# Kernel optimization log

Measured on AMD Instinct MI355X. Metric: run time of the kernel, lower is better.

Reference implementation:

```python
import jax, jax.numpy as jnp
import numpy as np

DIM = 1024
NUM_HEADS = 16
HEAD_DIM = DIM // NUM_HEADS
SCALE = HEAD_DIM ** -0.5


def setup_inputs() -> dict:
    key = jax.random.key(0)
    k1, k2, k3, k4 = jax.random.split(key, 4)
    x = jax.random.normal(k1, (4, 2048, DIM), dtype=jnp.float32)
    # torch nn.Linear(dim, 3*dim, bias=False): weight shape [3*dim, dim]
    w_qkv = jax.random.normal(k2, (3 * DIM, DIM), dtype=jnp.float32) * (DIM ** -0.5)
    # torch nn.Linear(dim, dim): weight [dim, dim], bias [dim]
    w_proj = jax.random.normal(k3, (DIM, DIM), dtype=jnp.float32) * (DIM ** -0.5)
    b_proj = jax.random.normal(k4, (DIM,), dtype=jnp.float32) * 0.01
    return {"x": x, "w_qkv": w_qkv, "w_proj": w_proj, "b_proj": b_proj}


def reference(x, w_qkv, w_proj, b_proj):
    B, N, C = x.shape
    # qkv: [B, N, 3*C] -> [3, B, H, N, Dh]
    qkv = (x @ w_qkv.T).reshape(B, N, 3, NUM_HEADS, HEAD_DIM)
    qkv = jnp.transpose(qkv, (2, 0, 3, 1, 4))
    q, k, v = qkv[0], qkv[1], qkv[2]
    # full score matrix, as in the original module
    attn = jnp.einsum("bhqd,bhkd->bhqk", q, k) * SCALE
    attn = jax.nn.softmax(attn, axis=-1)
    out = jnp.einsum("bhqk,bhkd->bhqd", attn, v)  # [B,H,N,Dh]
    out = jnp.transpose(out, (0, 2, 1, 3)).reshape(B, N, C)
    return out @ w_proj.T + b_proj
```

## Files before the change

### kernel.cpp

```cpp
#include <hip/hip_runtime.h>
#include <stdint.h>

#define DIM 1024
#define SEQ 2048
#define BATCH 4
#define ROWS (BATCH*SEQ)
#define QSCALE 0.1803368801111f

typedef __attribute__((ext_vector_type(8))) short bf16x8;
typedef __attribute__((ext_vector_type(4))) float f32x4;

#if __has_builtin(__builtin_amdgcn_exp2f)
#define EXP2F(x) __builtin_amdgcn_exp2f(x)
#else
#define EXP2F(x) __expf((x) * 0.69314718056f)
#endif

__device__ __forceinline__ unsigned short f2bf(float f) {
  union { float f; unsigned int u; } v; v.f = f;
  unsigned int u = v.u;
  return (unsigned short)((u + 0x7FFFu + ((u >> 16) & 1u)) >> 16);
}

__device__ __forceinline__ unsigned int pack_bf16_trunc(float lo, float hi) {
  union { float f; unsigned int u; } a, b;
  a.f = lo; b.f = hi;
  return __builtin_amdgcn_perm(b.u, a.u, 0x07060302u);
}

__device__ __forceinline__ void gload_lds16(const void* g, void* l) {
  __builtin_amdgcn_global_load_lds(
      (const __attribute__((address_space(1))) unsigned int*)g,
      (__attribute__((address_space(3))) unsigned int*)l,
      16, 0, 0);
}

__global__ void cast_f32_bf16(const float* __restrict__ src,
                              unsigned short* __restrict__ dst, int n) {
  int i = (blockIdx.x * blockDim.x + threadIdx.x) * 4;
  if (i < n) {
    float4 f = *(const float4*)(src + i);
    ushort4 o;
    o.x = f2bf(f.x); o.y = f2bf(f.y); o.z = f2bf(f.z); o.w = f2bf(f.w);
    *(ushort4*)(dst + i) = o;
  }
}

__global__ __launch_bounds__(256) void gemm_qkv(
    const unsigned short* __restrict__ A,
    const unsigned short* __restrict__ W,
    unsigned short* __restrict__ qb,
    unsigned short* __restrict__ kb,
    unsigned short* __restrict__ vtb) {
  const int K = DIM;
  __shared__ unsigned short Al[128 * 32];
  __shared__ unsigned short Wl[128 * 32];
  const int tid  = threadIdx.x;
  const int wave = tid >> 6, lane = tid & 63;
  const int quad = lane >> 4, l16 = lane & 15;
  const int m0 = blockIdx.y * 128, n0 = blockIdx.x * 128;
  const int wr = (wave >> 1) * 64, wc = (wave & 1) * 64;

  f32x4 acc[4][4];
#pragma unroll
  for (int i = 0; i < 4; i++)
#pragma unroll
    for (int j = 0; j < 4; j++) acc[i][j] = (f32x4)0.f;

  const int arow = wave * 16 + (lane >> 2);
  const int acol = (lane & 3) * 8;
  const unsigned short* Ag = A + (size_t)(m0 + arow) * K + acol;
  const unsigned short* Wg = W + (size_t)(n0 + arow) * K + acol;

  for (int kt = 0; kt < K; kt += 32) {
    __syncthreads();
#pragma unroll
    for (int i = 0; i < 2; i++) {
      gload_lds16((const void*)(Ag + (size_t)(i * 64) * K + kt), (void*)&Al[i * 2048 + wave * 512]);
      gload_lds16((const void*)(Wg + (size_t)(i * 64) * K + kt), (void*)&Wl[i * 2048 + wave * 512]);
    }
    __syncthreads();

    bf16x8 af[4], wf[4];
#pragma unroll
    for (int i = 0; i < 4; i++) {
      af[i] = *(const bf16x8*)&Al[(wr + i * 16 + l16) * 32 + quad * 8];
      wf[i] = *(const bf16x8*)&Wl[(wc + i * 16 + l16) * 32 + quad * 8];
    }
#pragma unroll
    for (int i = 0; i < 4; i++)
#pragma unroll
      for (int j = 0; j < 4; j++)
        acc[i][j] = __builtin_amdgcn_mfma_f32_16x16x32_bf16(af[i], wf[j], acc[i][j], 0, 0, 0);
  }

#pragma unroll
  for (int i = 0; i < 4; i++) {
    const int row = m0 + wr + i * 16 + quad * 4;
    const int b = row >> 11;
    const int n = row & 2047;
#pragma unroll
    for (int j = 0; j < 4; j++) {
      const int col = n0 + wc + j * 16 + l16;
      const int which = col >> 10;
      const int h = (col >> 6) & 15;
      const int d = col & 63;
      const int bh = b * 16 + h;
      if (which == 2) {
        ushort4 o4;
        o4.x = f2bf(acc[i][j][0]); o4.y = f2bf(acc[i][j][1]);
        o4.z = f2bf(acc[i][j][2]); o4.w = f2bf(acc[i][j][3]);
        *(ushort4*)&vtb[((size_t)bh * 64 + d) * SEQ + n] = o4;
      } else if (which == 0) {
        unsigned short* dst = qb + ((size_t)bh * SEQ + n) * 64 + d;
#pragma unroll
        for (int r = 0; r < 4; r++) dst[r * 64] = f2bf(acc[i][j][r] * QSCALE);
      } else {
        unsigned short* dst = kb + ((size_t)bh * SEQ + n) * 64 + d;
#pragma unroll
        for (int r = 0; r < 4; r++) dst[r * 64] = f2bf(acc[i][j][r]);
      }
    }
  }
}

__global__ __launch_bounds__(256, 2) void attn_kernel(
    const unsigned short* __restrict__ qb,
    const unsigned short* __restrict__ kb,
    const unsigned short* __restrict__ vtb,
    unsigned short* __restrict__ out) {
  __shared__ unsigned short Kl[64 * 64];
  __shared__ unsigned short Vl[64 * 64];
  __shared__ unsigned short Pb[4][64 * 64];

  const int tid  = threadIdx.x;
  const int wave = tid >> 6, lane = tid & 63;
  const int quad = lane >> 4, l16 = lane & 15;
  const int qtile = blockIdx.x;
  const int bh    = blockIdx.y;
  const size_t qkbase = (size_t)bh * SEQ * 64;
  const int q0 = qtile * 256 + wave * 64;

  bf16x8 qf[4][2];
#pragma unroll
  for (int mi = 0; mi < 4; mi++)
#pragma unroll
    for (int kk = 0; kk < 2; kk++)
      qf[mi][kk] = *(const bf16x8*)&qb[qkbase + (size_t)(q0 + mi * 16 + l16) * 64 + kk * 32 + quad * 8];

  f32x4 o[4][4];
#pragma unroll
  for (int mi = 0; mi < 4; mi++)
#pragma unroll
    for (int nt = 0; nt < 4; nt++) o[mi][nt] = (f32x4)0.f;
  f32x4 lacc[4];
#pragma unroll
  for (int mi = 0; mi < 4; mi++) lacc[mi] = (f32x4)0.f;

  bf16x8 ones;
#pragma unroll
  for (int j = 0; j < 8; j++) ones[j] = (short)0x3F80;

  const unsigned short* Kg = kb + qkbase;
  const unsigned short* Vg = vtb + (size_t)bh * 64 * SEQ;
  const int srow = tid >> 3;
  const int schk = tid & 7;

  for (int kt = 0; kt < SEQ; kt += 64) {
    __syncthreads();
#pragma unroll
    for (int p = 0; p < 2; p++) {
      const int r = p * 32 + srow;
      const int sw = schk ^ (r & 7);
      gload_lds16((const void*)(Kg + (size_t)(kt + r) * 64 + sw * 8),
                  (void*)&Kl[p * 2048 + wave * 512]);
      gload_lds16((const void*)(Vg + (size_t)r * SEQ + kt + sw * 8),
                  (void*)&Vl[p * 2048 + wave * 512]);
    }
    __syncthreads();

#pragma unroll
    for (int nh = 0; nh < 4; nh++) {
      const int R = nh * 16 + l16;
      const int sb = R & 7;
      bf16x8 kf0 = *(const bf16x8*)&Kl[R * 64 + ((quad ^ sb) << 3)];
      bf16x8 kf1 = *(const bf16x8*)&Kl[R * 64 + (((4 + quad) ^ sb) << 3)];
#pragma unroll
      for (int mi = 0; mi < 4; mi++) {
        f32x4 s = (f32x4)0.f;
        s = __builtin_amdgcn_mfma_f32_16x16x32_bf16(kf0, qf[mi][0], s, 0, 0, 0);
        s = __builtin_amdgcn_mfma_f32_16x16x32_bf16(kf1, qf[mi][1], s, 0, 0, 0);
        const float e0 = EXP2F(s[0]), e1 = EXP2F(s[1]);
        const float e2 = EXP2F(s[2]), e3 = EXP2F(s[3]);
        uint2 pk;
        pk.x = pack_bf16_trunc(e0, e1);
        pk.y = pack_bf16_trunc(e2, e3);
        const int q = mi * 16 + l16;
        const int chunk = (nh * 2 + (quad >> 1)) ^ (l16 & 7);
        *(uint2*)&Pb[wave][q * 64 + (chunk << 3) + ((quad & 1) << 2)] = pk;
      }
    }

#pragma unroll
    for (int kk = 0; kk < 2; kk++) {
      bf16x8 vf[4];
#pragma unroll
      for (int nt = 0; nt < 4; nt++) {
        const int R = nt * 16 + l16;
        vf[nt] = *(const bf16x8*)&Vl[R * 64 + (((kk * 4 + quad) ^ (R & 7)) << 3)];
      }
#pragma unroll
      for (int mi = 0; mi < 4; mi++) {
        const int R = mi * 16 + l16;
        bf16x8 pf = *(const bf16x8*)&Pb[wave][R * 64 + (((kk * 4 + quad) ^ (l16 & 7)) << 3)];
        lacc[mi] = __builtin_amdgcn_mfma_f32_16x16x32_bf16(pf, ones, lacc[mi], 0, 0, 0);
#pragma unroll
        for (int nt = 0; nt < 4; nt++)
          o[mi][nt] = __builtin_amdgcn_mfma_f32_16x16x32_bf16(pf, vf[nt], o[mi][nt], 0, 0, 0);
      }
    }
  }

  const int h = bh & 15, b = bh >> 4;
#pragma unroll
  for (int mi = 0; mi < 4; mi++) {
    float inv[4];
#pragma unroll
    for (int r = 0; r < 4; r++) inv[r] = 1.f / lacc[mi][r];
#pragma unroll
    for (int nt = 0; nt < 4; nt++)
#pragma unroll
      for (int r = 0; r < 4; r++)
        out[((size_t)(b * SEQ + q0 + mi * 16 + quad * 4 + r)) * DIM + h * 64 + nt * 16 + l16] =
            f2bf(o[mi][nt][r] * inv[r]);
  }
}

__global__ __launch_bounds__(256) void gemm_proj(
    const unsigned short* __restrict__ A,
    const unsigned short* __restrict__ W,
    float* __restrict__ out,
    const float* __restrict__ bias) {
  const int N = DIM, K = DIM;
  __shared__ unsigned short Al[128 * 32];
  __shared__ unsigned short Wl[128 * 32];
  const int tid  = threadIdx.x;
  const int wave = tid >> 6, lane = tid & 63;
  const int quad = lane >> 4, l16 = lane & 15;
  const int m0 = blockIdx.y * 128, n0 = blockIdx.x * 128;
  const int wr = (wave >> 1) * 64, wc = (wave & 1) * 64;

  f32x4 acc[4][4];
#pragma unroll
  for (int i = 0; i < 4; i++)
#pragma unroll
    for (int j = 0; j < 4; j++) acc[i][j] = (f32x4)0.f;

  const int arow = wave * 16 + (lane >> 2);
  const int acol = (lane & 3) * 8;
  const unsigned short* Ag = A + (size_t)(m0 + arow) * K + acol;
  const unsigned short* Wg = W + (size_t)(n0 + arow) * K + acol;

  for (int kt = 0; kt < K; kt += 32) {
    __syncthreads();
#pragma unroll
    for (int i = 0; i < 2; i++) {
      gload_lds16((const void*)(Ag + (size_t)(i * 64) * K + kt), (void*)&Al[i * 2048 + wave * 512]);
      gload_lds16((const void*)(Wg + (size_t)(i * 64) * K + kt), (void*)&Wl[i * 2048 + wave * 512]);
    }
    __syncthreads();

    bf16x8 af[4], wf[4];
#pragma unroll
    for (int i = 0; i < 4; i++) {
      af[i] = *(const bf16x8*)&Al[(wr + i * 16 + l16) * 32 + quad * 8];
      wf[i] = *(const bf16x8*)&Wl[(wc + i * 16 + l16) * 32 + quad * 8];
    }
#pragma unroll
    for (int i = 0; i < 4; i++)
#pragma unroll
      for (int j = 0; j < 4; j++)
        acc[i][j] = __builtin_amdgcn_mfma_f32_16x16x32_bf16(af[i], wf[j], acc[i][j], 0, 0, 0);
  }

#pragma unroll
  for (int i = 0; i < 4; i++) {
    const int row = m0 + wr + i * 16 + quad * 4;
#pragma unroll
    for (int j = 0; j < 4; j++) {
      const int col = n0 + wc + j * 16 + l16;
      const float bv = bias[col];
#pragma unroll
      for (int r = 0; r < 4; r++)
        out[(size_t)(row + r) * N + col] = acc[i][j][r] + bv;
    }
  }
}

extern "C" void kernel_launch(void* const* d_in, const int* in_sizes, int n_in,
                              void* d_out, int out_size, void* d_ws, size_t ws_size,
                              hipStream_t stream) {
  const float* x      = (const float*)d_in[0];
  const float* w_qkv  = (const float*)d_in[1];
  const float* w_proj = (const float*)d_in[2];
  const float* b_proj = (const float*)d_in[3];
  float* outp = (float*)d_out;

  char* ws = (char*)d_ws;
  unsigned short* xb     = (unsigned short*)(ws);
  unsigned short* wqkvb  = (unsigned short*)(ws + (16u << 20));
  unsigned short* wprojb = (unsigned short*)(ws + (22u << 20));
  unsigned short* qb     = (unsigned short*)(ws + (24u << 20));
  unsigned short* kb     = (unsigned short*)(ws + (40u << 20));
  unsigned short* vtb    = (unsigned short*)(ws + (56u << 20));
  unsigned short* aout   = (unsigned short*)(ws + (72u << 20));

  cast_f32_bf16<<<ROWS * DIM / 1024, 256, 0, stream>>>(x, xb, ROWS * DIM);
  cast_f32_bf16<<<3 * DIM * DIM / 1024, 256, 0, stream>>>(w_qkv, wqkvb, 3 * DIM * DIM);
  cast_f32_bf16<<<DIM * DIM / 1024, 256, 0, stream>>>(w_proj, wprojb, DIM * DIM);

  gemm_qkv<<<dim3(24, 64), 256, 0, stream>>>(xb, wqkvb, qb, kb, vtb);
  attn_kernel<<<dim3(8, 64), 256, 0, stream>>>(qb, kb, vtb, aout);
  gemm_proj<<<dim3(8, 64), 256, 0, stream>>>(aout, wprojb, outp, b_proj);
}
```

Measured before the change: 285.9 us.

## Double-buffer K/V tiles in attention and vectorize Q/K stores in QKV GEMM

The attention kernel now keeps two LDS buffers for the K and V tiles. It issues the global-to-LDS copy of the next 64-key tile right after the barrier, so the copy can run while the current tile is being computed. This also removes one barrier per iteration. In the QKV GEMM, blocks that produce Q or K swap the MFMA operand order so each lane's accumulator holds four consecutive head-dim values. That lets those blocks write packed ushort4 stores instead of four scattered 2-byte stores. The cost is doubled K/V LDS usage, 64KB per block, which is still meant to fit two blocks per CU. The GEMM main loop is now duplicated across the two branches.

```diff
diff --git a/kernel.cpp b/kernel.cpp
--- a/kernel.cpp
+++ b/kernel.cpp
@@ -60,6 +60,7 @@
   const int quad = lane >> 4, l16 = lane & 15;
   const int m0 = blockIdx.y * 128, n0 = blockIdx.x * 128;
   const int wr = (wave >> 1) * 64, wc = (wave & 1) * 64;
+  const int which = n0 >> 10;
 
   f32x4 acc[4][4];
 #pragma unroll
@@ -72,53 +73,76 @@
   const unsigned short* Ag = A + (size_t)(m0 + arow) * K + acol;
   const unsigned short* Wg = W + (size_t)(n0 + arow) * K + acol;
 
-  for (int kt = 0; kt < K; kt += 32) {
-    __syncthreads();
-#pragma unroll
-    for (int i = 0; i < 2; i++) {
-      gload_lds16((const void*)(Ag + (size_t)(i * 64) * K + kt), (void*)&Al[i * 2048 + wave * 512]);
-      gload_lds16((const void*)(Wg + (size_t)(i * 64) * K + kt), (void*)&Wl[i * 2048 + wave * 512]);
-    }
-    __syncthreads();
-
-    bf16x8 af[4], wf[4];
+  if (which < 2) {
+    for (int kt = 0; kt < K; kt += 32) {
+      __syncthreads();
+#pragma unroll
+      for (int i = 0; i < 2; i++) {
+        gload_lds16((const void*)(Ag + (size_t)(i * 64) * K + kt), (void*)&Al[i * 2048 + wave * 512]);
+        gload_lds16((const void*)(Wg + (size_t)(i * 64) * K + kt), (void*)&Wl[i * 2048 + wave * 512]);
+      }
+      __syncthreads();
+      bf16x8 af[4], wf[4];
+#pragma unroll
+      for (int i = 0; i < 4; i++) {
+        af[i] = *(const bf16x8*)&Al[(wr + i * 16 + l16) * 32 + quad * 8];
+        wf[i] = *(const bf16x8*)&Wl[(wc + i * 16 + l16) * 32 + quad * 8];
+      }
+#pragma unroll
+      for (int i = 0; i < 4; i++)
+#pragma unroll
+        for (int j = 0; j < 4; j++)
+          acc[i][j] = __builtin_amdgcn_mfma_f32_16x16x32_bf16(wf[j], af[i], acc[i][j], 0, 0, 0);
+    }
+    const float sc = (which == 0) ? QSCALE : 1.f;
+    unsigned short* base = (which == 0) ? qb : kb;
 #pragma unroll
     for (int i = 0; i < 4; i++) {
-      af[i] = *(const bf16x8*)&Al[(wr + i * 16 + l16) * 32 + quad * 8];
-      wf[i] = *(const bf16x8*)&Wl[(wc + i * 16 + l16) * 32 + quad * 8];
-    }
-#pragma unroll
-    for (int i = 0; i < 4; i++)
-#pragma unroll
-      for (int j = 0; j < 4; j++)
-        acc[i][j] = __builtin_amdgcn_mfma_f32_16x16x32_bf16(af[i], wf[j], acc[i][j], 0, 0, 0);
-  }
-
-#pragma unroll
-  for (int i = 0; i < 4; i++) {
-    const int row = m0 + wr + i * 16 + quad * 4;
-    const int b = row >> 11;
-    const int n = row & 2047;
-#pragma unroll
-    for (int j = 0; j < 4; j++) {
-      const int col = n0 + wc + j * 16 + l16;
-      const int which = col >> 10;
-      const int h = (col >> 6) & 15;
-      const int d = col & 63;
-      const int bh = b * 16 + h;
-      if (which == 2) {
+      const int tok = m0 + wr + i * 16 + l16;
+      const int b = tok >> 11, n = tok & 2047;
+#pragma unroll
+      for (int j = 0; j < 4; j++) {
+        const int col0 = n0 + wc + j * 16 + quad * 4;
+        const int h = (col0 >> 6) & 15, d = col0 & 63;
+        ushort4 o4;
+        o4.x = f2bf(acc[i][j][0] * sc); o4.y = f2bf(acc[i][j][1] * sc);
+        o4.z = f2bf(acc[i][j][2] * sc); o4.w = f2bf(acc[i][j][3] * sc);
+        *(ushort4*)&base[((size_t)(b * 16 + h) * SEQ + n) * 64 + d] = o4;
+      }
+    }
+  } else {
+    for (int kt = 0; kt < K; kt += 32) {
+      __syncthreads();
+#pragma unroll
+      for (int i = 0; i < 2; i++) {
+        gload_lds16((const void*)(Ag + (size_t)(i * 64) * K + kt), (void*)&Al[i * 2048 + wave * 512]);
+        gload_lds16((const void*)(Wg + (size_t)(i * 64) * K + kt), (void*)&Wl[i * 2048 + wave * 512]);
+      }
+      __syncthreads();
+      bf16x8 af[4], wf[4];
+#pragma unroll
+      for (int i = 0; i < 4; i++) {
+        af[i] = *(const bf16x8*)&Al[(wr + i * 16 + l16) * 32 + quad * 8];
+        wf[i] = *(const bf16x8*)&Wl[(wc + i * 16 + l16) * 32 + quad * 8];
+      }
+#pragma unroll
+      for (int i = 0; i < 4; i++)
+#pragma unroll
+        for (int j = 0; j < 4; j++)
+          acc[i][j] = __builtin_amdgcn_mfma_f32_16x16x32_bf16(af[i], wf[j], acc[i][j], 0, 0, 0);
+    }
+#pragma unroll
+    for (int i = 0; i < 4; i++) {
+      const int row = m0 + wr + i * 16 + quad * 4;
+      const int b = row >> 11, n = row & 2047;
+#pragma unroll
+      for (int j = 0; j < 4; j++) {
+        const int col = n0 + wc + j * 16 + l16;
+        const int h = (col >> 6) & 15, d = col & 63;
         ushort4 o4;
         o4.x = f2bf(acc[i][j][0]); o4.y = f2bf(acc[i][j][1]);
         o4.z = f2bf(acc[i][j][2]); o4.w = f2bf(acc[i][j][3]);
-        *(ushort4*)&vtb[((size_t)bh * 64 + d) * SEQ + n] = o4;
-      } else if (which == 0) {
-        unsigned short* dst = qb + ((size_t)bh * SEQ + n) * 64 + d;
-#pragma unroll
-        for (int r = 0; r < 4; r++) dst[r * 64] = f2bf(acc[i][j][r] * QSCALE);
-      } else {
-        unsigned short* dst = kb + ((size_t)bh * SEQ + n) * 64 + d;
-#pragma unroll
-        for (int r = 0; r < 4; r++) dst[r * 64] = f2bf(acc[i][j][r]);
+        *(ushort4*)&vtb[((size_t)(b * 16 + h) * 64 + d) * SEQ + n] = o4;
       }
     }
   }
@@ -129,8 +153,8 @@
     const unsigned short* __restrict__ kb,
     const unsigned short* __restrict__ vtb,
     unsigned short* __restrict__ out) {
-  __shared__ unsigned short Kl[64 * 64];
-  __shared__ unsigned short Vl[64 * 64];
+  __shared__ unsigned short Kl[2][64 * 64];
+  __shared__ unsigned short Vl[2][64 * 64];
   __shared__ unsigned short Pb[4][64 * 64];
 
   const int tid  = threadIdx.x;
@@ -166,25 +190,31 @@
   const int srow = tid >> 3;
   const int schk = tid & 7;
 
-  for (int kt = 0; kt < SEQ; kt += 64) {
-    __syncthreads();
+  auto stage = [&](int kt, int buf) {
 #pragma unroll
     for (int p = 0; p < 2; p++) {
       const int r = p * 32 + srow;
       const int sw = schk ^ (r & 7);
       gload_lds16((const void*)(Kg + (size_t)(kt + r) * 64 + sw * 8),
-                  (void*)&Kl[p * 2048 + wave * 512]);
+                  (void*)&Kl[buf][p * 2048 + wave * 512]);
       gload_lds16((const void*)(Vg + (size_t)r * SEQ + kt + sw * 8),
-                  (void*)&Vl[p * 2048 + wave * 512]);
-    }
+                  (void*)&Vl[buf][p * 2048 + wave * 512]);
+    }
+  };
+
+  stage(0, 0);
+
+  int buf = 0;
+  for (int kt = 0; kt < SEQ; kt += 64, buf ^= 1) {
     __syncthreads();
+    if (kt + 64 < SEQ) stage(kt + 64, buf ^ 1);
 
 #pragma unroll
     for (int nh = 0; nh < 4; nh++) {
       const int R = nh * 16 + l16;
       const int sb = R & 7;
-      bf16x8 kf0 = *(const bf16x8*)&Kl[R * 64 + ((quad ^ sb) << 3)];
-      bf16x8 kf1 = *(const bf16x8*)&Kl[R * 64 + (((4 + quad) ^ sb) << 3)];
+      bf16x8 kf0 = *(const bf16x8*)&Kl[buf][R * 64 + ((quad ^ sb) << 3)];
+      bf16x8 kf1 = *(const bf16x8*)&Kl[buf][R * 64 + (((4 + quad) ^ sb) << 3)];
 #pragma unroll
       for (int mi = 0; mi < 4; mi++) {
         f32x4 s = (f32x4)0.f;
@@ -207,7 +237,7 @@
 #pragma unroll
       for (int nt = 0; nt < 4; nt++) {
         const int R = nt * 16 + l16;
-        vf[nt] = *(const bf16x8*)&Vl[R * 64 + (((kk * 4 + quad) ^ (R & 7)) << 3)];
+        vf[nt] = *(const bf16x8*)&Vl[buf][R * 64 + (((kk * 4 + quad) ^ (R & 7)) << 3)];
       }
 #pragma unroll
       for (int mi = 0; mi < 4; mi++) {
```

Measured after the change: 266.2 us. -6.9%, faster.
